# Optimization experiments

Hardware: AMD Instinct MI355X
Metric: run time of the kernel (lower is better)

## Reference

```python
import jax, jax.numpy as jnp
import numpy as np

N_NODES = 100000
N_EDGES = 3200000
D = 256
L = 3
BN_EPS = 1e-5


def setup_inputs() -> dict:
    key = jax.random.key(0)
    ks = jax.random.split(key, 6)
    scale = 1.0 / np.sqrt(D)
    x = jax.random.normal(ks[0], (N_NODES, D), dtype=jnp.float32)
    W = jax.random.normal(ks[1], (L, D, D), dtype=jnp.float32) * scale
    b = jnp.zeros((L, D), dtype=jnp.float32)
    Wl = jax.random.normal(ks[2], (L, D, D), dtype=jnp.float32) * scale
    bl = jnp.zeros((L, D), dtype=jnp.float32)
    gamma = jnp.ones((L, D), dtype=jnp.float32)
    beta = jnp.zeros((L, D), dtype=jnp.float32)
    src = jax.random.randint(ks[3], (N_EDGES,), 0, N_NODES, dtype=jnp.int32)
    dst = jax.random.randint(ks[4], (N_EDGES,), 0, N_NODES, dtype=jnp.int32)
    return {"x": x, "W": W, "b": b, "Wl": Wl, "bl": bl,
            "gamma": gamma, "beta": beta, "src": src, "dst": dst}


def _gcn_head(x, W, b, Wl, bl, gamma, beta, src, dst):
    n = x.shape[0]
    ones = jnp.ones((src.shape[0],), dtype=x.dtype)
    # degrees (clamped to 1, as DGL GraphConv does)
    deg_out = jnp.maximum(jax.ops.segment_sum(ones, src, num_segments=n), 1.0)
    deg_in = jnp.maximum(jax.ops.segment_sum(ones, dst, num_segments=n), 1.0)
    inv_sqrt_out = (deg_out ** -0.5)[:, None]  # [N,1]
    inv_sqrt_in = (deg_in ** -0.5)[:, None]

    h = x
    for l in range(W.shape[0]):
        # GraphConv, norm='both': D_in^{-1/2} A D_out^{-1/2} h W + b
        hs = h * inv_sqrt_out
        agg = jax.ops.segment_sum(hs[src], dst, num_segments=n)  # [N,D]
        agg = agg * inv_sqrt_in
        out = agg @ W[l] + b[l]
        # residual + optional linear on the layer input
        out = out + h + (h @ Wl[l] + bl[l])
        # BatchNorm1d over nodes (training-style batch stats, biased var)
        mean = jnp.mean(out, axis=0)
        var = jnp.var(out, axis=0)
        out = gamma[l] * (out - mean) * jax.lax.rsqrt(var + BN_EPS) + beta[l]
        # ReLU (Dropout treated as identity / eval mode)
        h = jax.nn.relu(out)
    return h


def reference(x, W, b, Wl, bl, gamma, beta, src, dst):
    return _gcn_head(x, W, b, Wl, bl, gamma, beta, src, dst)
```

## Files before the change

### kernel.cpp

```cpp
#include <hip/hip_runtime.h>

#define D 256
#define BN_EPS 1e-5f

typedef __attribute__((ext_vector_type(8))) short short8;
typedef __attribute__((ext_vector_type(4))) float f32x4;
typedef __attribute__((ext_vector_type(2))) float f32x2;

__device__ __forceinline__ float b2f(ushort u) {
    union { unsigned u; float f; } c; c.u = ((unsigned)u) << 16; return c.f;
}
__device__ __forceinline__ ushort f2b(float f) {
    union { float f; unsigned u; } c; c.f = f;
    return (ushort)((c.u + 0x7fffu + ((c.u >> 16) & 1u)) >> 16);
}

typedef __attribute__((address_space(1))) const void gv_t;
typedef __attribute__((address_space(3))) void lv_t;
__device__ __forceinline__ void gld16(const void* g, void* l) {
    __builtin_amdgcn_global_load_lds((gv_t*)g, (lv_t*)l, 16, 0, 0);
}

__device__ __forceinline__ uint2 pk_fp8x8(const float* r) {
    unsigned w0 = 0, w1 = 0;
    w0 = __builtin_amdgcn_cvt_pk_fp8_f32(r[0], r[1], w0, false);
    w0 = __builtin_amdgcn_cvt_pk_fp8_f32(r[2], r[3], w0, true);
    w1 = __builtin_amdgcn_cvt_pk_fp8_f32(r[4], r[5], w1, false);
    w1 = __builtin_amdgcn_cvt_pk_fp8_f32(r[6], r[7], w1, true);
    return make_uint2(w0, w1);
}


#define HB 64

__global__ __launch_bounds__(256) void hist_kernel(const int* __restrict__ src,
                                                   const int* __restrict__ dst,
                                                   unsigned* __restrict__ P, int E) {
    __shared__ unsigned lhist[16384];
    int combo = blockIdx.y;
    const int* arr = (combo >> 2) ? dst : src;
    unsigned base = (unsigned)(combo & 3) << 15;
    for (int j = threadIdx.x; j < 16384; j += 256) lhist[j] = 0;
    __syncthreads();
    int i0 = (blockIdx.x * 256 + threadIdx.x) * 4;
    int stride = HB * 256 * 4;
    for (int i = i0; i < E; i += stride) {
        if (i + 3 < E) {
            int4 v = *(const int4*)(arr + i);
            unsigned r0 = (unsigned)v.x - base;
            unsigned r1 = (unsigned)v.y - base;
            unsigned r2 = (unsigned)v.z - base;
            unsigned r3 = (unsigned)v.w - base;
            if (r0 < 32768u) atomicAdd(&lhist[r0 >> 1], 1u << ((r0 & 1) << 4));
            if (r1 < 32768u) atomicAdd(&lhist[r1 >> 1], 1u << ((r1 & 1) << 4));
            if (r2 < 32768u) atomicAdd(&lhist[r2 >> 1], 1u << ((r2 & 1) << 4));
            if (r3 < 32768u) atomicAdd(&lhist[r3 >> 1], 1u << ((r3 & 1) << 4));
        } else {
            for (int j = i; j < E; j++) {
                unsigned r = (unsigned)arr[j] - base;
                if (r < 32768u) atomicAdd(&lhist[r >> 1], 1u << ((r & 1) << 4));
            }
        }
    }
    __syncthreads();
    unsigned* dstp = P + ((size_t)(combo * HB + blockIdx.x) << 14);
    for (int j = threadIdx.x; j < 16384; j += 256) dstp[j] = lhist[j];
}

__global__ void histreduce_kernel(const unsigned* __restrict__ P,
                                  int* __restrict__ cntO, int* __restrict__ cntI, int N) {
    int g = blockIdx.x * 256 + threadIdx.x;
    int array = g >> 16;
    int p = g & 65535;
    int range = p >> 14;
    int j = p & 16383;
    const unsigned* Pp = P + ((size_t)((array * 4 + range) * HB) << 14) + j;
    unsigned s = 0;
#pragma unroll 8
    for (int b = 0; b < HB; b++) s += Pp[(size_t)b << 14];
    int bin = (range << 15) + 2 * j;
    int* cnt = array ? cntI : cntO;
    if (bin < N)     cnt[bin]     = (int)(s & 0xFFFFu);
    if (bin + 1 < N) cnt[bin + 1] = (int)(s >> 16);
}

__global__ void invsqrt_kernel(const int* __restrict__ cntO, const int* __restrict__ cntI,
                               float* __restrict__ invO, float* __restrict__ invI,
                               float* __restrict__ sqrtO, int N) {
    int i = blockIdx.x * blockDim.x + threadIdx.x;
    if (i < N) {
        float dO = (float)max(cntO[i], 1);
        invO[i] = rsqrtf(dO);
        sqrtO[i] = sqrtf(dO);
        invI[i] = rsqrtf((float)max(cntI[i], 1));
    }
}

__global__ void scan1_kernel(const int* __restrict__ cnt, int* __restrict__ off,
                             int* __restrict__ bsum, int n) {
    __shared__ int s[256];
    int t = threadIdx.x;
    int i0 = blockIdx.x * 1024 + t * 4;
    int v0 = (i0 < n) ? ((cnt[i0] + 7) & ~7) : 0;
    int v1 = (i0 + 1 < n) ? ((cnt[i0 + 1] + 7) & ~7) : 0;
    int v2 = (i0 + 2 < n) ? ((cnt[i0 + 2] + 7) & ~7) : 0;
    int v3 = (i0 + 3 < n) ? ((cnt[i0 + 3] + 7) & ~7) : 0;
    int tsum = v0 + v1 + v2 + v3;
    s[t] = tsum;
    __syncthreads();
    for (int d = 1; d < 256; d <<= 1) {
        int x = (t >= d) ? s[t - d] : 0;
        __syncthreads();
        s[t] += x;
        __syncthreads();
    }
    int excl = s[t] - tsum;
    if (i0 < n)     off[i0]     = excl;
    if (i0 + 1 < n) off[i0 + 1] = excl + v0;
    if (i0 + 2 < n) off[i0 + 2] = excl + v0 + v1;
    if (i0 + 3 < n) off[i0 + 3] = excl + v0 + v1 + v2;
    if (t == 255) bsum[blockIdx.x] = s[255];
}

__global__ void scan2_kernel(int* __restrict__ bsum, int nb) {
    __shared__ int s[256];
    int t = threadIdx.x;
    int v = (t < nb) ? bsum[t] : 0;
    s[t] = v;
    __syncthreads();
    for (int d = 1; d < 256; d <<= 1) {
        int x = (t >= d) ? s[t - d] : 0;
        __syncthreads();
        s[t] += x;
        __syncthreads();
    }
    if (t < nb) bsum[t] = s[t] - v;
    if (t == nb - 1) bsum[1023] = s[t];
}

__global__ void scan3_kernel(int* __restrict__ off, const int* __restrict__ bsum,
                             int* __restrict__ bucketCur, int n) {
    int i = blockIdx.x * blockDim.x + threadIdx.x;
    if (i < n) {
        int v = off[i] + bsum[i >> 10];
        off[i] = v;
        if ((i & 255) == 0) bucketCur[i >> 8] = v;
    } else if (i == n) {
        off[n] = bsum[1023];
    }
}


#define NBKMAX 512

__global__ __launch_bounds__(256) void partA_kernel(const int* __restrict__ src,
                                                    const int* __restrict__ dst,
                                                    int* __restrict__ bucketCur,
                                                    unsigned* __restrict__ pairs,
                                                    int E, int NBK) {
    __shared__ int cnt[NBKMAX];
    __shared__ int base_s[NBKMAX];
    for (int j = threadIdx.x; j < NBK; j += 256) cnt[j] = 0;
    __syncthreads();
    for (int i = blockIdx.x * 256 + threadIdx.x; i < E; i += gridDim.x * 256)
        atomicAdd(&cnt[((unsigned)dst[i]) >> 8], 1);
    __syncthreads();
    for (int j = threadIdx.x; j < NBK; j += 256) {
        base_s[j] = atomicAdd(&bucketCur[j], cnt[j]);
        cnt[j] = 0;
    }
    __syncthreads();
    for (int i = blockIdx.x * 256 + threadIdx.x; i < E; i += gridDim.x * 256) {
        unsigned d = (unsigned)dst[i];
        unsigned b = d >> 8;
        int pos = base_s[b] + atomicAdd(&cnt[b], 1);
        pairs[pos] = ((unsigned)src[i] << 8) | (d & 255u);
    }
}

#define BCAP 14336

__global__ __launch_bounds__(256) void partB_kernel(const unsigned* __restrict__ pairs,
                                                    const int* __restrict__ off,
                                                    const int* __restrict__ bucketCur,
                                                    int* __restrict__ srcS, int N) {
    __shared__ int curL[256];
    __shared__ int stage[BCAP];
    int b = blockIdx.x;
    int n0 = b << 8;
    int n1 = min(n0 + 256, N);
    int base = off[n0];
    int len = off[n1] - base;
    if (len > BCAP) len = BCAP;
    for (int j = threadIdx.x; j < len; j += 256) stage[j] = N;
    int nn = n1 - n0;
    for (int i = threadIdx.x; i < nn; i += 256) curL[i] = off[n0 + i] - base;
    __syncthreads();
    int cntB = bucketCur[b] - base;
    for (int j = threadIdx.x; j < cntB; j += 256) {
        unsigned p = pairs[base + j];
        int pos = atomicAdd(&curL[p & 255u], 1);
        if (pos < BCAP) stage[pos] = (int)(p >> 8);
    }
    __syncthreads();
    for (int j4 = threadIdx.x; j4 * 4 < len; j4 += 256)
        *(int4*)(srcS + base + j4 * 4) = *(const int4*)(stage + j4 * 4);
}

__global__ void init_pad_kernel(ushort* __restrict__ X, unsigned* __restrict__ X8, int N) {
    int t = threadIdx.x;
    X[(size_t)N * D + t] = 0;
    if (t < 64) X8[(size_t)N * 64 + t] = 0;
}


__global__ void prep_w_kernel(const float* __restrict__ W, const float* __restrict__ Wl,
                              const float* __restrict__ b, const float* __restrict__ bl,
                              ushort* __restrict__ Wt, float* __restrict__ bcat, int L) {
    int idx = blockIdx.x * blockDim.x + threadIdx.x;
    int k = idx & 511;
    int n = (idx >> 9) & 255;
    int l = idx >> 17;
    if (l >= L) return;
    float v;
    if (k < 256) {
        v = W[(size_t)l * 65536 + k * 256 + n];
    } else {
        v = Wl[(size_t)l * 65536 + (k - 256) * 256 + n];
        if (k - 256 == n) v += 1.0f;
    }
    Wt[idx] = f2b(v);
    if (k == 0) bcat[l * 256 + n] = b[l * 256 + n] + bl[l * 256 + n];
}

__global__ void x2b_kernel(const float* __restrict__ x, const float* __restrict__ invO,
                           ushort* __restrict__ hs, unsigned* __restrict__ hs8, long n8) {
    long i8 = (long)blockIdx.x * blockDim.x + threadIdx.x;
    if (i8 >= n8) return;
    long row = i8 >> 5;
    float sc = invO[row];
    float4 a = ((const float4*)x)[i8 * 2];
    float4 b = ((const float4*)x)[i8 * 2 + 1];
    float r[8] = { a.x * sc, a.y * sc, a.z * sc, a.w * sc,
                   b.x * sc, b.y * sc, b.z * sc, b.w * sc };
    ushort v[8];
#pragma unroll
    for (int j = 0; j < 8; j++) v[j] = f2b(r[j]);
    *(short8*)(hs + i8 * 8) = *(short8*)v;
    *(uint2*)(hs8 + i8 * 2) = pk_fp8x8(r);
}


__global__ void aggregate_kernel(const unsigned* __restrict__ hs8, const float* __restrict__ invO,
                                 const float* __restrict__ invI, const int* __restrict__ off,
                                 const int* __restrict__ srcS, ushort* __restrict__ aggs, int N) {
    int node = (blockIdx.x * blockDim.x + threadIdx.x) >> 6;
    int lane = threadIdx.x & 63;
    if (node >= N) return;
    int e0 = off[node], e1 = off[node + 1];
    float a0 = 0.f, a1 = 0.f, a2 = 0.f, a3 = 0.f;
    for (int e = e0; e < e1; e += 8) {
        int4 c0 = *(const int4*)(srcS + e);
        int4 c1 = *(const int4*)(srcS + e + 4);
        unsigned g0 = hs8[(size_t)c0.x * 64 + lane];
        unsigned g1 = hs8[(size_t)c0.y * 64 + lane];
        unsigned g2 = hs8[(size_t)c0.z * 64 + lane];
        unsigned g3 = hs8[(size_t)c0.w * 64 + lane];
        unsigned g4 = hs8[(size_t)c1.x * 64 + lane];
        unsigned g5 = hs8[(size_t)c1.y * 64 + lane];
        unsigned g6 = hs8[(size_t)c1.z * 64 + lane];
        unsigned g7 = hs8[(size_t)c1.w * 64 + lane];
#pragma unroll
        for (int q = 0; q < 8; q++) {
            unsigned g = (q == 0) ? g0 : (q == 1) ? g1 : (q == 2) ? g2 : (q == 3) ? g3
                       : (q == 4) ? g4 : (q == 5) ? g5 : (q == 6) ? g6 : g7;
            f32x2 lo = __builtin_amdgcn_cvt_pk_f32_fp8(g, false);
            f32x2 hi = __builtin_amdgcn_cvt_pk_f32_fp8(g, true);
            a0 += lo[0]; a1 += lo[1]; a2 += hi[0]; a3 += hi[1];
        }
    }
    float wi = invI[node] * invO[node];
    ushort4 o;
    o.x = f2b(a0 * wi); o.y = f2b(a1 * wi); o.z = f2b(a2 * wi); o.w = f2b(a3 * wi);
    *(ushort4*)(aggs + (size_t)node * D + lane * 4) = o;
}


__global__ __launch_bounds__(256) void gemm_kernel(
        const ushort* __restrict__ aggs, const ushort* __restrict__ hs,
        const ushort* __restrict__ Wt,  const float* __restrict__ bcat,
        const float* __restrict__ sqrtO,
        ushort* __restrict__ tmp, float* __restrict__ bnsum, float* __restrict__ bnsq,
        int M) {
    __shared__ short As[128 * 32];
    __shared__ short Bs[128 * 32];

    int bid = blockIdx.x;
    int bm = (bid & 7) + (bid >> 4) * 8;
    int bn0 = ((bid >> 3) & 1) * 128;
    if (bm * 128 >= M) return;
    int bm0 = bm * 128;

    int tid = threadIdx.x;
    int wid = tid >> 6, lane = tid & 63;
    int wr = wid >> 1, wc = wid & 1;
    int lrow = lane & 15, lkh = lane >> 4;
    int srow = lane >> 2;
    int sseg = (lane & 3) ^ ((srow >> 1) & 3);

    f32x4 acc[4][4] = {};

    for (int k0 = 0; k0 < 512; k0 += 32) {
        int kk = k0 & 255;
        const ushort* Ahalf = (k0 < 256) ? aggs : hs;
        const ushort* ga0 = Ahalf + (size_t)(bm0 + wid * 32 + srow) * 256 + kk + sseg * 8;
        const ushort* gb0 = Wt + (size_t)(bn0 + wid * 32 + srow) * 512 + k0 + sseg * 8;
        gld16(ga0,            &As[(wid * 32) * 32]);
        gld16(ga0 + 16 * 256, &As[(wid * 32 + 16) * 32]);
        gld16(gb0,            &Bs[(wid * 32) * 32]);
        gld16(gb0 + 16 * 512, &Bs[(wid * 32 + 16) * 32]);
        __syncthreads();

        short8 a[4], bfr[4];
#pragma unroll
        for (int m = 0; m < 4; m++) {
            int ra = wr * 64 + m * 16 + lrow;
            a[m] = *(short8*)&As[ra * 32 + (lkh ^ ((ra >> 1) & 3)) * 8];
        }
#pragma unroll
        for (int n = 0; n < 4; n++) {
            int rb = wc * 64 + n * 16 + lrow;
            bfr[n] = *(short8*)&Bs[rb * 32 + (lkh ^ ((rb >> 1) & 3)) * 8];
        }
#pragma unroll
        for (int m = 0; m < 4; m++)
#pragma unroll
            for (int n = 0; n < 4; n++)
                acc[m][n] = __builtin_amdgcn_mfma_f32_16x16x32_bf16(a[m], bfr[n], acc[m][n], 0, 0, 0);
        __syncthreads();
    }

#pragma unroll
    for (int n = 0; n < 4; n++) {
        int col = bn0 + wc * 64 + n * 16 + lrow;
        float bc = bcat[col];
        float s_part = 0.f, q_part = 0.f;
#pragma unroll
        for (int m = 0; m < 4; m++) {
            int rbase = bm0 + wr * 64 + m * 16 + lkh * 4;
#pragma unroll
            for (int i = 0; i < 4; i++) {
                int row = rbase + i;
                if (row < M) {
                    float v = acc[m][n][i] * sqrtO[row] + bc;
                    tmp[(size_t)row * D + col] = f2b(v);
                    s_part += v;
                    q_part += v * v;
                }
            }
        }
        s_part += __shfl_xor(s_part, 16);
        s_part += __shfl_xor(s_part, 32);
        q_part += __shfl_xor(q_part, 16);
        q_part += __shfl_xor(q_part, 32);
        if (lkh == 0) {
            atomicAdd(&bnsum[col], s_part);
            atomicAdd(&bnsq[col], q_part);
        }
    }
}


__global__ void bnfin_kernel(float* __restrict__ bnsum, float* __restrict__ bnsq,
                             const float* __restrict__ gamma, const float* __restrict__ beta,
                             float2* __restrict__ bnab, float invM) {
    int c = threadIdx.x;
    float mean = bnsum[c] * invM;
    float var = bnsq[c] * invM - mean * mean;
    float a = gamma[c] * rsqrtf(var + BN_EPS);
    bnab[c] = make_float2(a, beta[c] - a * mean);
    bnsum[c] = 0.f;
    bnsq[c] = 0.f;
}

__global__ void bnrelu_kernel(const ushort* __restrict__ tmp, const float2* __restrict__ bnab,
                              const float* __restrict__ invO, ushort* __restrict__ Xout,
                              unsigned* __restrict__ X8out, float* __restrict__ out,
                              int M, int last) {
    long i8 = (long)blockIdx.x * blockDim.x + threadIdx.x;
    if (i8 >= (long)M * 32) return;
    long row = i8 >> 5;
    int c0 = ((int)(i8 & 31)) * 8;
    short8 v = *(const short8*)(tmp + row * D + c0);
    float r[8];
#pragma unroll
    for (int j = 0; j < 8; j++) {
        float2 ab = bnab[c0 + j];
        float x = b2f((ushort)v[j]);
        r[j] = fmaxf(ab.x * x + ab.y, 0.f);
    }
    if (last) {
        float4 f0 = make_float4(r[0], r[1], r[2], r[3]);
        float4 f1 = make_float4(r[4], r[5], r[6], r[7]);
        ((float4*)(out + row * D + c0))[0] = f0;
        ((float4*)(out + row * D + c0))[1] = f1;
    } else {
        float sc = invO[row];
        ushort w[8];
#pragma unroll
        for (int j = 0; j < 8; j++) { r[j] *= sc; w[j] = f2b(r[j]); }
        *(short8*)(Xout + row * D + c0) = *(short8*)w;
        *(uint2*)(X8out + i8 * 2) = pk_fp8x8(r);
    }
}


extern "C" void kernel_launch(void* const* d_in, const int* in_sizes, int n_in,
                              void* d_out, int out_size, void* d_ws, size_t ws_size,
                              hipStream_t stream) {
    const float* x     = (const float*)d_in[0];
    const float* W     = (const float*)d_in[1];
    const float* b     = (const float*)d_in[2];
    const float* Wl    = (const float*)d_in[3];
    const float* bl    = (const float*)d_in[4];
    const float* gamma = (const float*)d_in[5];
    const float* beta  = (const float*)d_in[6];
    const int*   src   = (const int*)d_in[7];
    const int*   dst   = (const int*)d_in[8];

    const int N = in_sizes[0] / D;
    const int E = in_sizes[7];
    const int L = in_sizes[1] / (D * D);
    const int M_pad = (N + 1 + 127) & ~127;
    const int E_pad = E + 7 * N + 64;
    const int NBK = (N + 255) >> 8;
    float* out = (float*)d_out;

    char* p = (char*)d_ws;
    auto alloc = [&](size_t bytes) -> char* {
        char* r = p;
        p += (bytes + 255) & ~(size_t)255;
        return r;
    };
    int*      cur   = (int*)alloc((size_t)NBKMAX * 4);
    int*      cntO  = (int*)alloc((size_t)N * 4);
    int*      cntI  = (int*)alloc((size_t)N * 4);
    float*    invO  = (float*)alloc((size_t)(N + 1) * 4);
    float*    invI  = (float*)alloc((size_t)N * 4);
    float*    sqrtO = (float*)alloc((size_t)(N + 1) * 4);
    int*      off_  = (int*)alloc((size_t)(N + 1) * 4);
    int*      bsum  = (int*)alloc(1024 * 4);
    int*      srcS  = (int*)alloc((size_t)E_pad * 4);
    ushort*   Wt    = (ushort*)alloc((size_t)L * 256 * 512 * 2);
    float*    bcat  = (float*)alloc((size_t)L * 256 * 4);
    ushort*   X     = (ushort*)alloc((size_t)M_pad * D * 2);
    unsigned* X8    = (unsigned*)alloc((size_t)M_pad * 64 * 4);
    ushort*   aggs  = (ushort*)alloc((size_t)M_pad * D * 2);
    ushort*   tmp   = (ushort*)alloc((size_t)M_pad * D * 2);
    float*    bnsum = (float*)alloc((size_t)2 * D * 4);
    float*    bnsq  = bnsum + D;
    float2*   bnab  = (float2*)alloc((size_t)D * 8);

    unsigned* P     = (unsigned*)aggs;
    unsigned* pairs = (unsigned*)aggs;

    {
        dim3 hg(HB, 8);
        hist_kernel<<<hg, 256, 0, stream>>>(src, dst, P, E);
        histreduce_kernel<<<512, 256, 0, stream>>>(P, cntO, cntI, N);
    }
    invsqrt_kernel<<<(N + 255) / 256, 256, 0, stream>>>(cntO, cntI, invO, invI, sqrtO, N);
    int NB = (N + 1023) / 1024;
    scan1_kernel<<<NB, 256, 0, stream>>>(cntI, off_, bsum, N);
    scan2_kernel<<<1, 256, 0, stream>>>(bsum, NB);
    scan3_kernel<<<(N + 256) / 256, 256, 0, stream>>>(off_, bsum, cur, N);
    partA_kernel<<<512, 256, 0, stream>>>(src, dst, cur, pairs, E, NBK);
    partB_kernel<<<NBK, 256, 0, stream>>>(pairs, off_, cur, srcS, N);
    init_pad_kernel<<<1, 256, 0, stream>>>(X, X8, N);

    prep_w_kernel<<<(L * 256 * 512 + 255) / 256, 256, 0, stream>>>(W, Wl, b, bl, Wt, bcat, L);
    x2b_kernel<<<(int)(((long)N * 32 + 255) / 256), 256, 0, stream>>>(x, invO, X, X8, (long)N * 32);
    hipMemsetAsync(bnsum, 0, 2 * D * sizeof(float), stream);

    const int MB = (N + 127) / 128;
    const int gemm_grid = ((MB + 7) >> 3) * 16;
    const float invM = 1.0f / (float)N;
    for (int l = 0; l < L; l++) {
        int last = (l == L - 1);

        aggregate_kernel<<<(N + 3) / 4, 256, 0, stream>>>(X8, invO, invI, off_, srcS, aggs, N);

        gemm_kernel<<<gemm_grid, 256, 0, stream>>>(aggs, X, Wt + (size_t)l * 256 * 512,
                                                   bcat + l * 256, sqrtO, tmp, bnsum, bnsq, N);

        bnfin_kernel<<<1, 256, 0, stream>>>(bnsum, bnsq, gamma + l * D, beta + l * D, bnab, invM);
        bnrelu_kernel<<<(int)(((long)N * 32 + 255) / 256), 256, 0, stream>>>(
            tmp, bnab, invO, X, X8, out, N, last);
    }
}
```

Before: 828.4 us.

## Split fp8 feature table into column halves and aggregate each half separately

Reorganizes the fp8 node-feature table into two contiguous column halves of 128 bytes per row, and runs the gather-aggregate kernel twice, once per half, with each half-wave handling one node. Each pass gathers from a table half the size, which is meant to fit the random-access working set better into L2/MALL cache. The per-node in/out degree scale is also precomputed as a single product array. The cost is double the index-list reads and two kernel launches per layer.

```diff
diff --git a/kernel.cpp b/kernel.cpp
--- a/kernel.cpp
+++ b/kernel.cpp
@@ -85,14 +85,15 @@
 }
 
 __global__ void invsqrt_kernel(const int* __restrict__ cntO, const int* __restrict__ cntI,
-                               float* __restrict__ invO, float* __restrict__ invI,
+                               float* __restrict__ invO, float* __restrict__ invOI,
                                float* __restrict__ sqrtO, int N) {
     int i = blockIdx.x * blockDim.x + threadIdx.x;
     if (i < N) {
         float dO = (float)max(cntO[i], 1);
-        invO[i] = rsqrtf(dO);
+        float io = rsqrtf(dO);
+        invO[i] = io;
         sqrtO[i] = sqrtf(dO);
-        invI[i] = rsqrtf((float)max(cntI[i], 1));
+        invOI[i] = io * rsqrtf((float)max(cntI[i], 1));
     }
 }
 
@@ -207,10 +208,11 @@
         *(int4*)(srcS + base + j4 * 4) = *(const int4*)(stage + j4 * 4);
 }
 
-__global__ void init_pad_kernel(ushort* __restrict__ X, unsigned* __restrict__ X8, int N) {
+__global__ void init_pad_kernel(ushort* __restrict__ X, unsigned* __restrict__ X8,
+                                int N, long strideH) {
     int t = threadIdx.x;
     X[(size_t)N * D + t] = 0;
-    if (t < 64) X8[(size_t)N * 64 + t] = 0;
+    if (t < 64) X8[(t >> 5) * strideH + (size_t)N * 32 + (t & 31)] = 0;
 }
 
 
@@ -234,7 +236,8 @@
 }
 
 __global__ void x2b_kernel(const float* __restrict__ x, const float* __restrict__ invO,
-                           ushort* __restrict__ hs, unsigned* __restrict__ hs8, long n8) {
+                           ushort* __restrict__ hs, unsigned* __restrict__ hs8,
+                           long strideH, long n8) {
     long i8 = (long)blockIdx.x * blockDim.x + threadIdx.x;
     if (i8 >= n8) return;
     long row = i8 >> 5;
@@ -247,42 +250,50 @@
 #pragma unroll
     for (int j = 0; j < 8; j++) v[j] = f2b(r[j]);
     *(short8*)(hs + i8 * 8) = *(short8*)v;
-    *(uint2*)(hs8 + i8 * 2) = pk_fp8x8(r);
-}
-
-
-__global__ void aggregate_kernel(const unsigned* __restrict__ hs8, const float* __restrict__ invO,
-                                 const float* __restrict__ invI, const int* __restrict__ off,
-                                 const int* __restrict__ srcS, ushort* __restrict__ aggs, int N) {
-    int node = (blockIdx.x * blockDim.x + threadIdx.x) >> 6;
-    int lane = threadIdx.x & 63;
-    if (node >= N) return;
-    int e0 = off[node], e1 = off[node + 1];
-    float a0 = 0.f, a1 = 0.f, a2 = 0.f, a3 = 0.f;
+    long H = (i8 >> 4) & 1;
+    *(uint2*)(hs8 + H * strideH + row * 32 + (i8 & 15) * 2) = pk_fp8x8(r);
+}
+
+
+__global__ void aggregate_kernel(const unsigned* __restrict__ hs8h,
+                                 const float* __restrict__ invOI,
+                                 const int* __restrict__ off, const int* __restrict__ srcS,
+                                 ushort* __restrict__ aggsh, int N) {
+    int tid = threadIdx.x;
+    int wid = tid >> 6, lane = tid & 63;
+    int l32 = lane & 31;
+    int node = blockIdx.x * 8 + wid * 2 + (lane >> 5);
+    if (blockIdx.x * 8 + wid * 2 >= N) return;
+    bool valid = node < N;
+    int e0 = valid ? off[node] : 0;
+    int e1 = valid ? off[node + 1] : 0;
+    f32x2 A01 = {0.f, 0.f}, A23 = {0.f, 0.f};
     for (int e = e0; e < e1; e += 8) {
         int4 c0 = *(const int4*)(srcS + e);
         int4 c1 = *(const int4*)(srcS + e + 4);
-        unsigned g0 = hs8[(size_t)c0.x * 64 + lane];
-        unsigned g1 = hs8[(size_t)c0.y * 64 + lane];
-        unsigned g2 = hs8[(size_t)c0.z * 64 + lane];
-        unsigned g3 = hs8[(size_t)c0.w * 64 + lane];
-        unsigned g4 = hs8[(size_t)c1.x * 64 + lane];
-        unsigned g5 = hs8[(size_t)c1.y * 64 + lane];
-        unsigned g6 = hs8[(size_t)c1.z * 64 + lane];
-        unsigned g7 = hs8[(size_t)c1.w * 64 + lane];
+        unsigned g0 = hs8h[(size_t)c0.x * 32 + l32];
+        unsigned g1 = hs8h[(size_t)c0.y * 32 + l32];
+        unsigned g2 = hs8h[(size_t)c0.z * 32 + l32];
+        unsigned g3 = hs8h[(size_t)c0.w * 32 + l32];
+        unsigned g4 = hs8h[(size_t)c1.x * 32 + l32];
+        unsigned g5 = hs8h[(size_t)c1.y * 32 + l32];
+        unsigned g6 = hs8h[(size_t)c1.z * 32 + l32];
+        unsigned g7 = hs8h[(size_t)c1.w * 32 + l32];
 #pragma unroll
         for (int q = 0; q < 8; q++) {
             unsigned g = (q == 0) ? g0 : (q == 1) ? g1 : (q == 2) ? g2 : (q == 3) ? g3
                        : (q == 4) ? g4 : (q == 5) ? g5 : (q == 6) ? g6 : g7;
-            f32x2 lo = __builtin_amdgcn_cvt_pk_f32_fp8(g, false);
-            f32x2 hi = __builtin_amdgcn_cvt_pk_f32_fp8(g, true);
-            a0 += lo[0]; a1 += lo[1]; a2 += hi[0]; a3 += hi[1];
+            A01 += __builtin_amdgcn_cvt_pk_f32_fp8(g, false);
+            A23 += __builtin_amdgcn_cvt_pk_f32_fp8(g, true);
         }
     }
-    float wi = invI[node] * invO[node];
-    ushort4 o;
-    o.x = f2b(a0 * wi); o.y = f2b(a1 * wi); o.z = f2b(a2 * wi); o.w = f2b(a3 * wi);
-    *(ushort4*)(aggs + (size_t)node * D + lane * 4) = o;
+    if (valid) {
+        float wi = invOI[node];
+        ushort4 o;
+        o.x = f2b(A01[0] * wi); o.y = f2b(A01[1] * wi);
+        o.z = f2b(A23[0] * wi); o.w = f2b(A23[1] * wi);
+        *(ushort4*)(aggsh + (size_t)node * D + l32 * 4) = o;
+    }
 }
 
 
@@ -385,8 +396,8 @@
 
 __global__ void bnrelu_kernel(const ushort* __restrict__ tmp, const float2* __restrict__ bnab,
                               const float* __restrict__ invO, ushort* __restrict__ Xout,
-                              unsigned* __restrict__ X8out, float* __restrict__ out,
-                              int M, int last) {
+                              unsigned* __restrict__ X8out, long strideH,
+                              float* __restrict__ out, int M, int last) {
     long i8 = (long)blockIdx.x * blockDim.x + threadIdx.x;
     if (i8 >= (long)M * 32) return;
     long row = i8 >> 5;
@@ -410,7 +421,8 @@
 #pragma unroll
         for (int j = 0; j < 8; j++) { r[j] *= sc; w[j] = f2b(r[j]); }
         *(short8*)(Xout + row * D + c0) = *(short8*)w;
-        *(uint2*)(X8out + i8 * 2) = pk_fp8x8(r);
+        long H = (i8 >> 4) & 1;
+        *(uint2*)(X8out + H * strideH + row * 32 + (i8 & 15) * 2) = pk_fp8x8(r);
     }
 }
 
@@ -434,6 +446,7 @@
     const int M_pad = (N + 1 + 127) & ~127;
     const int E_pad = E + 7 * N + 64;
     const int NBK = (N + 255) >> 8;
+    const long strideH = (long)M_pad * 32;
     float* out = (float*)d_out;
 
     char* p = (char*)d_ws;
@@ -446,7 +459,7 @@
     int*      cntO  = (int*)alloc((size_t)N * 4);
     int*      cntI  = (int*)alloc((size_t)N * 4);
     float*    invO  = (float*)alloc((size_t)(N + 1) * 4);
-    float*    invI  = (float*)alloc((size_t)N * 4);
+    float*    invOI = (float*)alloc((size_t)(N + 1) * 4);
     float*    sqrtO = (float*)alloc((size_t)(N + 1) * 4);
     int*      off_  = (int*)alloc((size_t)(N + 1) * 4);
     int*      bsum  = (int*)alloc(1024 * 4);
@@ -454,7 +467,7 @@
     ushort*   Wt    = (ushort*)alloc((size_t)L * 256 * 512 * 2);
     float*    bcat  = (float*)alloc((size_t)L * 256 * 4);
     ushort*   X     = (ushort*)alloc((size_t)M_pad * D * 2);
-    unsigned* X8    = (unsigned*)alloc((size_t)M_pad * 64 * 4);
+    unsigned* X8    = (unsigned*)alloc((size_t)2 * strideH * 4);
     ushort*   aggs  = (ushort*)alloc((size_t)M_pad * D * 2);
     ushort*   tmp   = (ushort*)alloc((size_t)M_pad * D * 2);
     float*    bnsum = (float*)alloc((size_t)2 * D * 4);
@@ -469,32 +482,36 @@
         hist_kernel<<<hg, 256, 0, stream>>>(src, dst, P, E);
         histreduce_kernel<<<512, 256, 0, stream>>>(P, cntO, cntI, N);
     }
-    invsqrt_kernel<<<(N + 255) / 256, 256, 0, stream>>>(cntO, cntI, invO, invI, sqrtO, N);
+    invsqrt_kernel<<<(N + 255) / 256, 256, 0, stream>>>(cntO, cntI, invO, invOI, sqrtO, N);
     int NB = (N + 1023) / 1024;
     scan1_kernel<<<NB, 256, 0, stream>>>(cntI, off_, bsum, N);
     scan2_kernel<<<1, 256, 0, stream>>>(bsum, NB);
     scan3_kernel<<<(N + 256) / 256, 256, 0, stream>>>(off_, bsum, cur, N);
     partA_kernel<<<512, 256, 0, stream>>>(src, dst, cur, pairs, E, NBK);
     partB_kernel<<<NBK, 256, 0, stream>>>(pairs, off_, cur, srcS, N);
-    init_pad_kernel<<<1, 256, 0, stream>>>(X, X8, N);
+    init_pad_kernel<<<1, 256, 0, stream>>>(X, X8, N, strideH);
 
     prep_w_kernel<<<(L * 256 * 512 + 255) / 256, 256, 0, stream>>>(W, Wl, b, bl, Wt, bcat, L);
-    x2b_kernel<<<(int)(((long)N * 32 + 255) / 256), 256, 0, stream>>>(x, invO, X, X8, (long)N * 32);
+    x2b_kernel<<<(int)(((long)N * 32 + 255) / 256), 256, 0, stream>>>(
+        x, invO, X, X8, strideH, (long)N * 32);
     hipMemsetAsync(bnsum, 0, 2 * D * sizeof(float), stream);
 
     const int MB = (N + 127) / 128;
     const int gemm_grid = ((MB + 7) >> 3) * 16;
+    const int agg_grid = (N + 7) / 8;
     const float invM = 1.0f / (float)N;
     for (int l = 0; l < L; l++) {
         int last = (l == L - 1);
 
-        aggregate_kernel<<<(N + 3) / 4, 256, 0, stream>>>(X8, invO, invI, off_, srcS, aggs, N);
+        aggregate_kernel<<<agg_grid, 256, 0, stream>>>(X8, invOI, off_, srcS, aggs, N);
+        aggregate_kernel<<<agg_grid, 256, 0, stream>>>(X8 + strideH, invOI, off_, srcS,
+                                                       aggs + 128, N);
 
         gemm_kernel<<<gemm_grid, 256, 0, stream>>>(aggs, X, Wt + (size_t)l * 256 * 512,
                                                    bcat + l * 256, sqrtO, tmp, bnsum, bnsq, N);
 
         bnfin_kernel<<<1, 256, 0, stream>>>(bnsum, bnsq, gamma + l * D, beta + l * D, bnab, invM);
         bnrelu_kernel<<<(int)(((long)N * 32 + 255) / 256), 256, 0, stream>>>(
-            tmp, bnab, invO, X, X8, out, N, last);
-    }
-}
+            tmp, bnab, invO, X, X8, strideH, out, N, last);
+    }
+}
```

After: 816.5 us. About the same (-1.4%).
